# Performance work log

Hardware: AMD Instinct MI355X
Metric: run time of the kernel (lower is better)

Reference implementation:

```python
import jax, jax.numpy as jnp
import numpy as np

B, T, D, H = 8, 1024, 512, 8
HD = D // H  # head_dim = 64


def conv1d(x, w, b):
    # x: [B, C_in, T], w: [C_out, C_in, 3], 'same' padding
    y = jax.lax.conv_general_dilated(x, w, (1,), [(1, 1)],
                                     dimension_numbers=('NCH', 'OIH', 'NCH'))
    return y + b[None, :, None]


def setup_inputs() -> dict:
    key = jax.random.key(0)
    ks = jax.random.split(key, 9)
    s = 0.05
    return {
        'x': jax.random.normal(ks[0], (B, T, D), dtype=jnp.float32),
        'w11': jax.random.normal(ks[1], (D, D, 3), dtype=jnp.float32) * s,
        'b11': jnp.zeros((D,), dtype=jnp.float32),
        'w12': jax.random.normal(ks[2], (D, D, 3), dtype=jnp.float32) * s,
        'b12': jnp.zeros((D,), dtype=jnp.float32),
        'w13': jax.random.normal(ks[3], (D, D, 3), dtype=jnp.float32) * s,
        'b13': jnp.zeros((D,), dtype=jnp.float32),
        'w2': jax.random.normal(ks[4], (D, 2 * D, 3), dtype=jnp.float32) * s,
        'b2': jnp.zeros((D,), dtype=jnp.float32),
    }


def reference(x, w11, b11, w12, b12, w13, b13, w2, b2):
    # dropout is identity in eval mode
    b, t, d = x.shape
    xc = jnp.transpose(x, (0, 2, 1))  # [B, D, T]

    def proj(w, bb):
        y = jax.nn.relu(conv1d(xc, w, bb))        # [B, D, T]
        y = jnp.transpose(y, (0, 2, 1))           # [B, T, D]
        return y.reshape(b, t, H, HD)             # [B, T, H, HD]

    q = proj(w11, b11)
    k = proj(w12, b12)
    v = proj(w13, b13)

    # ---- time-wise attention (d_k = head_dim) ----
    qf = jnp.transpose(q, (0, 2, 1, 3))  # [B, H, T, HD]
    kf = jnp.transpose(k, (0, 2, 1, 3))
    vf = jnp.transpose(v, (0, 2, 1, 3))
    sf = jnp.einsum('bhtd,bhsd->bhts', qf, kf) / np.sqrt(HD)  # [B,H,T,T]
    af = jax.nn.softmax(sf, axis=-1)
    valuesf = jnp.einsum('bhts,bhsd->bhtd', af, vf)           # [B,H,T,HD]
    valuesf = jnp.transpose(valuesf, (0, 2, 1, 3)).reshape(b, t, H * HD)

    # ---- channel-wise attention (d_k = T, scores over head_dim) ----
    qt = jnp.transpose(q, (0, 2, 3, 1))  # [B, H, HD, T]
    kt = jnp.transpose(k, (0, 2, 3, 1))
    vt = jnp.transpose(v, (0, 2, 3, 1))
    st = jnp.einsum('bhct,bhdt->bhcd', qt, kt) / np.sqrt(t)   # [B,H,HD,HD]
    at = jax.nn.softmax(st, axis=-1)
    valuest = jnp.einsum('bhcd,bhdt->bhct', at, vt)           # [B,H,HD,T]
    # torch: permute(0,2,3,1).reshape(B, T, H*HD)
    valuest = jnp.transpose(valuest, (0, 2, 3, 1)).reshape(b, t, H * HD)

    values = jnp.concatenate([valuesf, valuest], axis=-1)     # [B, T, 2D]
    values = jnp.transpose(values, (0, 2, 1))                 # [B, 2D, T]
    out = jax.nn.relu(conv1d(values, w2, b2))                 # [B, D, T]
    return jnp.transpose(out, (0, 2, 1))                      # [B, T, D]
```

## Files before the change

kernel.cpp:

```cpp
#include <hip/hip_runtime.h>

#define BB 8
#define TT 1024
#define DD 512
#define DD2 1024
#define HH 8
#define HDIM 64
#define TP (TT + 2)

typedef short short8 __attribute__((ext_vector_type(8)));
typedef float floatx4 __attribute__((ext_vector_type(4)));

typedef const __attribute__((address_space(1))) unsigned int* gas_ptr;
typedef __attribute__((address_space(3))) unsigned int* las_ptr;

__device__ __forceinline__ unsigned short f2bf(float f) {
    union { float f; unsigned u; } v; v.f = f;
    unsigned r = v.u + 0x7fffu + ((v.u >> 16) & 1u);
    return (unsigned short)(r >> 16);
}

__device__ __forceinline__ void gl2lds16(const void* g, void* l) {
    __builtin_amdgcn_global_load_lds((gas_ptr)g, (las_ptr)l, 16, 0, 0);
}

#define NX4BLK 4104
#define NW1BLK 9216
#define NW2BLK 6144
#define NZBLK 1024
__global__ void k_prep(const float* __restrict__ x, const float* __restrict__ w0,
                       const float* __restrict__ w1, const float* __restrict__ w2,
                       const float* __restrict__ wo,
                       unsigned short* __restrict__ xp, unsigned short* __restrict__ wqkv,
                       unsigned short* __restrict__ w2k, unsigned short* __restrict__ vp,
                       float* __restrict__ gbuf) {
    int blk = blockIdx.x;
    if (blk < NX4BLK) {
        int idx = blk * 256 + threadIdx.x;
        int c4 = idx % (DD / 4);
        int rt = idx / (DD / 4);
        int row = rt % TP;
        int b = rt / TP;
        ushort4 o = {0, 0, 0, 0};
        if (row >= 1 && row <= TT) {
            float4 vv = *(const float4*)&x[((size_t)(b * TT + row - 1)) * DD + c4 * 4];
            o.x = f2bf(vv.x); o.y = f2bf(vv.y); o.z = f2bf(vv.z); o.w = f2bf(vv.w);
        }
        *(ushort4*)&xp[(size_t)idx * 4] = o;
        return;
    }
    blk -= NX4BLK;
    if (blk < NW1BLK) {
        int idx = blk * 256 + threadIdx.x;
        int e = idx & 7;
        int lane = (idx >> 3) & 63;
        int co0 = (idx >> 9) & 31;
        int ci0 = (idx >> 14) & 15;
        int rest = idx >> 18;
        int k = rest % 3, p = rest / 3;
        int co = co0 * 16 + (lane & 15);
        int ci = ci0 * 32 + (lane >> 4) * 8 + e;
        const float* w = (p == 0) ? w0 : ((p == 1) ? w1 : w2);
        wqkv[idx] = f2bf(w[(co * DD + ci) * 3 + k]);
        return;
    }
    blk -= NW1BLK;
    if (blk < NW2BLK) {
        int idx = blk * 256 + threadIdx.x;
        int e = idx & 7;
        int lane = (idx >> 3) & 63;
        int co0 = (idx >> 9) & 31;
        int ci0 = (idx >> 14) & 31;
        int k = idx >> 19;
        int co = co0 * 16 + (lane & 15);
        int ci = ci0 * 32 + (lane >> 4) * 8 + e;
        w2k[idx] = f2bf(wo[(co * DD2 + ci) * 3 + k]);
        return;
    }
    blk -= NW2BLK;
    {
        int idx = blk * 256 + threadIdx.x;
        if (idx < BB * 2 * 2 * DD) {
            int c = idx % (2 * DD);
            int t1 = idx / (2 * DD);
            int row = (t1 & 1) ? (TT + 1) : 0;
            int b = t1 >> 1;
            vp[(b * TP + row) * (2 * DD) + c] = 0;
        }
        if (idx < 64 * HDIM * HDIM) gbuf[idx] = 0.f;
    }
}

__global__ __launch_bounds__(256) void k_qkv_conv(
    const unsigned short* __restrict__ xp, const unsigned short* __restrict__ wfrag,
    const float* __restrict__ b11, const float* __restrict__ b12, const float* __restrict__ b13,
    unsigned short* __restrict__ q, unsigned short* __restrict__ qt,
    unsigned short* __restrict__ kfrag, unsigned short* __restrict__ kt,
    unsigned short* __restrict__ v, unsigned short* __restrict__ vtfrag) {
    __shared__ short As[2][80 * 32];
    int wave = threadIdx.x >> 6, lane = threadIdx.x & 63;
    int l15 = lane & 15, quad = lane >> 4;
    int tb = blockIdx.x * 64;
    int cb = blockIdx.y * 128;
    int proj = blockIdx.z % 3, b = blockIdx.z / 3;
    const short* A = (const short*)xp + b * TP * DD;
    const short* WF = (const short*)wfrag + (size_t)proj * 786432 + lane * 8;
    int srow = lane >> 2;
    int scs = (((lane & 3) ^ ((lane >> 3) & 3)) << 3);
    int co0b = (cb >> 4) + wave * 2;

    floatx4 acc[4][2];
#pragma unroll
    for (int mi = 0; mi < 4; ++mi)
#pragma unroll
        for (int ni = 0; ni < 2; ++ni) acc[mi][ni] = (floatx4){0.f, 0.f, 0.f, 0.f};

    auto stage = [&](int it) {
        short* dst = As[it & 1];
        int cib = it * 32;
        for (int j = wave; j < 5; j += 4)
            gl2lds16(A + (tb + j * 16 + srow) * DD + cib + scs, &dst[j * 512]);
    };

    stage(0);
    __syncthreads();

    for (int it = 0; it < 16; ++it) {
        if (it < 15) stage(it + 1);
        const short* Asb = As[it & 1];
        short8 bf[3][2];
#pragma unroll
        for (int k = 0; k < 3; ++k)
#pragma unroll
            for (int ni = 0; ni < 2; ++ni)
                bf[k][ni] = *(const short8*)(WF + ((size_t)((k * 16 + it) * 32 + co0b + ni) << 9));
#pragma unroll
        for (int k = 0; k < 3; ++k) {
            short8 af[4];
#pragma unroll
            for (int mi = 0; mi < 4; ++mi) {
                int arow = mi * 16 + l15 + k;
                af[mi] = *(const short8*)&Asb[arow * 32 + ((quad ^ ((arow >> 1) & 3)) << 3)];
            }
#pragma unroll
            for (int mi = 0; mi < 4; ++mi)
#pragma unroll
                for (int ni = 0; ni < 2; ++ni)
                    acc[mi][ni] = __builtin_amdgcn_mfma_f32_16x16x32_bf16(af[mi], bf[k][ni], acc[mi][ni], 0, 0, 0);
        }
        __syncthreads();
    }

    const float* bias = (proj == 0) ? b11 : ((proj == 1) ? b12 : b13);
#pragma unroll
    for (int ni = 0; ni < 2; ++ni) {
        int co = cb + wave * 32 + ni * 16 + l15;
        float bv = bias[co];
        int h = co >> 6, hd = co & 63;
        int bh = b * HH + h;
#pragma unroll
        for (int mi = 0; mi < 4; ++mi) {
            int tbase = tb + mi * 16 + quad * 4;
            unsigned short bb[4];
            ushort4 pk;
#pragma unroll
            for (int r = 0; r < 4; ++r) {
                float val = fmaxf(acc[mi][ni][r] + bv, 0.f);
                bb[r] = f2bf(val);
                ((unsigned short*)&pk)[r] = bb[r];
            }
            if (proj == 0) {
#pragma unroll
                for (int r = 0; r < 4; ++r)
                    q[((size_t)bh * TT + tbase + r) * HDIM + hd] = bb[r];
                *(ushort4*)&qt[((size_t)bh * HDIM + hd) * TT + tbase] = pk;
            } else if (proj == 1) {
                *(ushort4*)&kt[((size_t)bh * HDIM + hd) * TT + tbase] = pk;
                int sblk = tbase >> 6;
                int jr = (quad & 1) + 2 * (mi >> 1);
                int l15a_base = 4 * (quad >> 1) + 8 * (mi & 1);
                int kf = hd >> 5, quad_a = (hd >> 3) & 3, elem = hd & 7;
                size_t base = ((((size_t)bh * 16 + sblk) * 4 + jr) * 2 + kf) * 512 +
                              quad_a * 128 + elem;
#pragma unroll
                for (int r = 0; r < 4; ++r)
                    kfrag[base + (l15a_base + r) * 8] = bb[r];
            } else {
#pragma unroll
                for (int r = 0; r < 4; ++r)
                    v[((size_t)bh * TT + tbase + r) * HDIM + hd] = bb[r];
                int sblk = tbase >> 6;
                int df = hd >> 4, l15a = hd & 15;
                int kf = mi >> 1;
                int quad_a = 2 * (mi & 1) + (quad >> 1);
                int elem = (quad & 1) * 4;
                size_t base = ((((size_t)bh * 16 + sblk) * 4 + df) * 2 + kf) * 512 +
                              (quad_a * 16 + l15a) * 8 + elem;
                *(ushort4*)&vtfrag[base] = pk;
            }
        }
    }
}

__global__ __launch_bounds__(256) void k_attn_gram(
    const unsigned short* __restrict__ q, const unsigned short* __restrict__ kfrag,
    const unsigned short* __restrict__ vtfrag, const unsigned short* __restrict__ qt,
    const unsigned short* __restrict__ kt, float* __restrict__ gbuf,
    unsigned short* __restrict__ vp) {
    int wave = threadIdx.x >> 6, lane = threadIdx.x & 63;
    int l15 = lane & 15, quad = lane >> 4;
    int bh = blockIdx.y;

    if (blockIdx.x < 16) {
        int b = bh >> 3, h = bh & 7;
        int qr = blockIdx.x * 64 + wave * 16;
        const short* Q = (const short*)q + (size_t)bh * TT * HDIM;
        const short* KF = (const short*)kfrag + (size_t)bh * 16 * 8 * 512 + lane * 8;
        const short* VF = (const short*)vtfrag + (size_t)bh * 16 * 8 * 512 + lane * 8;

        short8 bq[2];
#pragma unroll
        for (int kf = 0; kf < 2; ++kf)
            bq[kf] = *(const short8*)(Q + (qr + l15) * HDIM + kf * 32 + quad * 8);

        floatx4 o[4];
#pragma unroll
        for (int df = 0; df < 4; ++df) o[df] = (floatx4){0.f, 0.f, 0.f, 0.f};
        float lacc = 0.f;

        for (int sblk = 0; sblk < 16; ++sblk) {
            const short* kp = KF + sblk * 8 * 512;
            const short* vv = VF + sblk * 8 * 512;
            floatx4 c[4];
#pragma unroll
            for (int jr = 0; jr < 4; ++jr) c[jr] = (floatx4){0.f, 0.f, 0.f, 0.f};
#pragma unroll
            for (int jr = 0; jr < 4; ++jr) {
#pragma unroll
                for (int kf = 0; kf < 2; ++kf) {
                    short8 ak = *(const short8*)(kp + (jr * 2 + kf) * 512);
                    c[jr] = __builtin_amdgcn_mfma_f32_16x16x32_bf16(ak, bq[kf], c[jr], 0, 0, 0);
                }
            }
            short8 pb[2];
#pragma unroll
            for (int kf = 0; kf < 2; ++kf) {
                union { short8 s; unsigned u[4]; } pk;
#pragma unroll
                for (int half = 0; half < 2; ++half) {
                    floatx4 cc = c[2 * kf + half];
                    float p0 = __expf(cc[0] * 0.125f);
                    float p1 = __expf(cc[1] * 0.125f);
                    float p2 = __expf(cc[2] * 0.125f);
                    float p3 = __expf(cc[3] * 0.125f);
                    lacc += (p0 + p1) + (p2 + p3);
                    pk.u[half * 2] =
                        __builtin_amdgcn_perm(__float_as_uint(p1), __float_as_uint(p0), 0x07060302u);
                    pk.u[half * 2 + 1] =
                        __builtin_amdgcn_perm(__float_as_uint(p3), __float_as_uint(p2), 0x07060302u);
                }
                pb[kf] = pk.s;
            }
#pragma unroll
            for (int df = 0; df < 4; ++df) {
#pragma unroll
                for (int kf = 0; kf < 2; ++kf) {
                    short8 av = *(const short8*)(vv + (df * 2 + kf) * 512);
                    o[df] = __builtin_amdgcn_mfma_f32_16x16x32_bf16(av, pb[kf], o[df], 0, 0, 0);
                }
            }
        }

        lacc += __shfl_xor(lacc, 16);
        lacc += __shfl_xor(lacc, 32);
        float linv = 1.f / lacc;

        unsigned short* vrow = vp + (size_t)(b * TP + 1 + qr + l15) * (2 * DD) + h * 64;
#pragma unroll
        for (int df = 0; df < 4; ++df) {
            ushort4 pk;
#pragma unroll
            for (int r = 0; r < 4; ++r) ((unsigned short*)&pk)[r] = f2bf(o[df][r] * linv);
            *(ushort4*)&vrow[df * 16 + quad * 4] = pk;
        }
    } else {
        int tc = blockIdx.x - 16;
        const short* Qt = (const short*)qt + (size_t)bh * HDIM * TT;
        const short* Kt = (const short*)kt + (size_t)bh * HDIM * TT;

        floatx4 g[4];
#pragma unroll
        for (int nt = 0; nt < 4; ++nt) g[nt] = (floatx4){0.f, 0.f, 0.f, 0.f};

        int t0b = tc * 256;
        for (int t0 = 0; t0 < 256; t0 += 32) {
            short8 aq = *(const short8*)(Qt + (wave * 16 + l15) * TT + t0b + t0 + quad * 8);
#pragma unroll
            for (int nt = 0; nt < 4; ++nt) {
                short8 bk = *(const short8*)(Kt + (nt * 16 + l15) * TT + t0b + t0 + quad * 8);
                g[nt] = __builtin_amdgcn_mfma_f32_16x16x32_bf16(aq, bk, g[nt], 0, 0, 0);
            }
        }
        float* gb = gbuf + bh * HDIM * HDIM;
#pragma unroll
        for (int nt = 0; nt < 4; ++nt) {
#pragma unroll
            for (int r = 0; r < 4; ++r) {
                int row = wave * 16 + quad * 4 + r;
                atomicAdd(&gb[row * HDIM + nt * 16 + l15], g[nt][r]);
            }
        }
    }
}

__global__ __launch_bounds__(256) void k_chan_av(
    const float* __restrict__ gbuf, const unsigned short* __restrict__ v,
    unsigned short* __restrict__ vp) {
    __shared__ short lds_a[64 * 64];
    int wave = threadIdx.x >> 6, lane = threadIdx.x & 63;
    int l15 = lane & 15, quad = lane >> 4;
    int tc = blockIdx.x, bh = blockIdx.y;
    int b = bh >> 3, h = bh & 7;
    const float sc = 0.03125f;

    if (threadIdx.x < 64) {
        const float* gb = gbuf + bh * HDIM * HDIM + threadIdx.x * HDIM;
        float mx = -3.0e38f;
        for (int j = 0; j < 64; ++j) mx = fmaxf(mx, gb[j] * sc);
        float sum = 0.f;
        for (int j = 0; j < 64; ++j) sum += __expf(gb[j] * sc - mx);
        float inv = 1.f / sum;
        for (int j = 0; j < 64; ++j)
            lds_a[threadIdx.x * 64 + j] = (short)f2bf(__expf(gb[j] * sc - mx) * inv);
    }
    __syncthreads();

    const short* V = (const short*)v + (size_t)bh * TT * HDIM;
    short8 pa[2];
#pragma unroll
    for (int kf = 0; kf < 2; ++kf)
        pa[kf] = *(const short8*)&lds_a[(wave * 16 + l15) * 64 + kf * 32 + quad * 8];

    for (int tt = 0; tt < 16; ++tt) {
        int ttile = tc * 16 + tt;
        floatx4 c = (floatx4){0.f, 0.f, 0.f, 0.f};
#pragma unroll
        for (int kf = 0; kf < 2; ++kf) {
            short8 bv = *(const short8*)(V + (ttile * 16 + l15) * HDIM + kf * 32 + quad * 8);
            c = __builtin_amdgcn_mfma_f32_16x16x32_bf16(pa[kf], bv, c, 0, 0, 0);
        }
        int t = ttile * 16 + l15;
#pragma unroll
        for (int r = 0; r < 4; ++r) {
            int crow = wave * 16 + quad * 4 + r;
            int tout = crow * 16 + (t >> 6);
            int col = 512 + ((t & 63) << 3) + h;
            vp[(b * TP + 1 + tout) * (2 * DD) + col] = f2bf(c[r]);
        }
    }
}

__global__ __launch_bounds__(256) void k_out_conv(
    const unsigned short* __restrict__ vp, const unsigned short* __restrict__ w2k,
    const float* __restrict__ b2, float* __restrict__ out) {
    __shared__ short As[2][144 * 64];
    int wave = threadIdx.x >> 6, lane = threadIdx.x & 63;
    int l15 = lane & 15, quad = lane >> 4;
    int wm = wave >> 1, wn = wave & 1;
    int tb = blockIdx.x * 128;
    int cb = blockIdx.y * 64;
    int b = blockIdx.z;
    const short* A = (const short*)vp + b * TP * DD2;
    const short* WF = (const short*)w2k + lane * 8;
    int srow8 = lane >> 3;
    int scl = ((lane & 7) ^ srow8) * 8;
    int co0b = (cb >> 4) + wn * 2;

    floatx4 acc[4][2];
#pragma unroll
    for (int mi = 0; mi < 4; ++mi)
#pragma unroll
        for (int ni = 0; ni < 2; ++ni) acc[mi][ni] = (floatx4){0.f, 0.f, 0.f, 0.f};

    auto stage = [&](int it) {
        short* dst = As[it & 1];
        int cib = it * 64;
        for (int g = wave; g < 18; g += 4) {
            int j = g >> 1, hf = g & 1;
            int row = hf * 8 + srow8;
            gl2lds16(A + (tb + j * 16 + row) * DD2 + cib + scl, &dst[j * 1024 + hf * 512]);
        }
    };

    stage(0);
    __syncthreads();

    for (int it = 0; it < 16; ++it) {
        if (it < 15) stage(it + 1);
        const short* Asb = As[it & 1];
#pragma unroll
        for (int k = 0; k < 3; ++k) {
            short8 bf[2][2];
#pragma unroll
            for (int kfh = 0; kfh < 2; ++kfh)
#pragma unroll
                for (int ni = 0; ni < 2; ++ni)
                    bf[kfh][ni] = *(const short8*)(WF +
                        ((size_t)((k * 32 + it * 2 + kfh) * 32 + co0b + ni) << 9));
#pragma unroll
            for (int kfh = 0; kfh < 2; ++kfh) {
                short8 af[4];
#pragma unroll
                for (int mi = 0; mi < 4; ++mi) {
                    int arow = wm * 64 + mi * 16 + l15 + k;
                    int cl = kfh * 4 + quad;
                    af[mi] = *(const short8*)&Asb[arow * 64 + ((cl ^ (arow & 7)) << 3)];
                }
#pragma unroll
                for (int mi = 0; mi < 4; ++mi)
#pragma unroll
                    for (int ni = 0; ni < 2; ++ni)
                        acc[mi][ni] = __builtin_amdgcn_mfma_f32_16x16x32_bf16(af[mi], bf[kfh][ni], acc[mi][ni], 0, 0, 0);
            }
        }
        __syncthreads();
    }

#pragma unroll
    for (int ni = 0; ni < 2; ++ni) {
        int co = cb + wn * 32 + ni * 16 + l15;
        float bv = b2[co];
#pragma unroll
        for (int mi = 0; mi < 4; ++mi) {
#pragma unroll
            for (int r = 0; r < 4; ++r) {
                int t = tb + wm * 64 + mi * 16 + quad * 4 + r;
                out[((size_t)b * TT + t) * DD + co] = fmaxf(acc[mi][ni][r] + bv, 0.f);
            }
        }
    }
}

extern "C" void kernel_launch(void* const* d_in, const int* in_sizes, int n_in,
                              void* d_out, int out_size, void* d_ws, size_t ws_size,
                              hipStream_t stream) {
    const float* x = (const float*)d_in[0];
    const float* w11 = (const float*)d_in[1];
    const float* b11 = (const float*)d_in[2];
    const float* w12 = (const float*)d_in[3];
    const float* b12 = (const float*)d_in[4];
    const float* w13 = (const float*)d_in[5];
    const float* b13 = (const float*)d_in[6];
    const float* w2 = (const float*)d_in[7];
    const float* b2 = (const float*)d_in[8];
    float* out = (float*)d_out;

    char* ws = (char*)d_ws;
    size_t off = 0;
    auto alloc = [&](size_t bytes) {
        void* p = ws + off;
        off += (bytes + 255) & ~(size_t)255;
        return p;
    };
    unsigned short* xp = (unsigned short*)alloc((size_t)BB * TP * DD * 2);
    unsigned short* wqkv = (unsigned short*)alloc((size_t)9 * DD * DD * 2);
    unsigned short* w2k = (unsigned short*)alloc((size_t)3 * DD * DD2 * 2);
    unsigned short* q = (unsigned short*)alloc((size_t)BB * HH * TT * HDIM * 2);
    unsigned short* qt = (unsigned short*)alloc((size_t)BB * HH * TT * HDIM * 2);
    unsigned short* kfrag = (unsigned short*)alloc((size_t)BB * HH * TT * HDIM * 2);
    unsigned short* kt = (unsigned short*)alloc((size_t)BB * HH * TT * HDIM * 2);
    unsigned short* v = (unsigned short*)alloc((size_t)BB * HH * TT * HDIM * 2);
    unsigned short* vtfrag = (unsigned short*)alloc((size_t)BB * HH * TT * HDIM * 2);
    float* gbuf = (float*)alloc((size_t)64 * HDIM * HDIM * 4);
    unsigned short* vp = (unsigned short*)alloc((size_t)BB * TP * 2 * DD * 2);
    (void)alloc(65536);

    k_prep<<<NX4BLK + NW1BLK + NW2BLK + NZBLK, 256, 0, stream>>>(x, w11, w12, w13, w2,
                                                                 xp, wqkv, w2k, vp, gbuf);
    k_qkv_conv<<<dim3(TT / 64, DD / 128, BB * 3), 256, 0, stream>>>(xp, wqkv, b11, b12, b13,
                                                                    q, qt, kfrag, kt, v, vtfrag);
    k_attn_gram<<<dim3(20, BB * HH), 256, 0, stream>>>(q, kfrag, vtfrag, qt, kt, gbuf, vp);
    k_chan_av<<<dim3(4, BB * HH), 256, 0, stream>>>(gbuf, v, vp);
    k_out_conv<<<dim3(TT / 128, DD / 64, BB), 256, 0, stream>>>(vp, w2k, b2, out);
}
```

Measured before the change: 236.2 us.

## Double time tile in QKV conv and stage K/V fragments through LDS in attention

The QKV conv kernel now computes 128 time steps per block instead of 64, so each wave reuses its weight fragments across eight M-tiles, and the fragment index math is adjusted to match. The time-wise attention branch now double-buffers K and V fragment blocks in shared memory with async global-to-LDS loads, replacing direct global reads shared by the four waves. This aims to cut weight and K/V global traffic. In exchange it uses more registers and LDS, launches fewer conv blocks, and adds a barrier on every attention iteration.

```diff
diff --git a/kernel.cpp b/kernel.cpp
--- a/kernel.cpp
+++ b/kernel.cpp
@@ -97,10 +97,10 @@
     unsigned short* __restrict__ q, unsigned short* __restrict__ qt,
     unsigned short* __restrict__ kfrag, unsigned short* __restrict__ kt,
     unsigned short* __restrict__ v, unsigned short* __restrict__ vtfrag) {
-    __shared__ short As[2][80 * 32];
+    __shared__ short As[2][144 * 32];
     int wave = threadIdx.x >> 6, lane = threadIdx.x & 63;
     int l15 = lane & 15, quad = lane >> 4;
-    int tb = blockIdx.x * 64;
+    int tb = blockIdx.x * 128;
     int cb = blockIdx.y * 128;
     int proj = blockIdx.z % 3, b = blockIdx.z / 3;
     const short* A = (const short*)xp + b * TP * DD;
@@ -109,16 +109,16 @@
     int scs = (((lane & 3) ^ ((lane >> 3) & 3)) << 3);
     int co0b = (cb >> 4) + wave * 2;
 
-    floatx4 acc[4][2];
-#pragma unroll
-    for (int mi = 0; mi < 4; ++mi)
+    floatx4 acc[8][2];
+#pragma unroll
+    for (int mi = 0; mi < 8; ++mi)
 #pragma unroll
         for (int ni = 0; ni < 2; ++ni) acc[mi][ni] = (floatx4){0.f, 0.f, 0.f, 0.f};
 
     auto stage = [&](int it) {
         short* dst = As[it & 1];
         int cib = it * 32;
-        for (int j = wave; j < 5; j += 4)
+        for (int j = wave; j < 9; j += 4)
             gl2lds16(A + (tb + j * 16 + srow) * DD + cib + scs, &dst[j * 512]);
     };
 
@@ -136,17 +136,13 @@
                 bf[k][ni] = *(const short8*)(WF + ((size_t)((k * 16 + it) * 32 + co0b + ni) << 9));
 #pragma unroll
         for (int k = 0; k < 3; ++k) {
-            short8 af[4];
-#pragma unroll
-            for (int mi = 0; mi < 4; ++mi) {
+#pragma unroll
+            for (int mi = 0; mi < 8; ++mi) {
                 int arow = mi * 16 + l15 + k;
-                af[mi] = *(const short8*)&Asb[arow * 32 + ((quad ^ ((arow >> 1) & 3)) << 3)];
-            }
-#pragma unroll
-            for (int mi = 0; mi < 4; ++mi)
-#pragma unroll
-                for (int ni = 0; ni < 2; ++ni)
-                    acc[mi][ni] = __builtin_amdgcn_mfma_f32_16x16x32_bf16(af[mi], bf[k][ni], acc[mi][ni], 0, 0, 0);
+                short8 af = *(const short8*)&Asb[arow * 32 + ((quad ^ ((arow >> 1) & 3)) << 3)];
+                acc[mi][0] = __builtin_amdgcn_mfma_f32_16x16x32_bf16(af, bf[k][0], acc[mi][0], 0, 0, 0);
+                acc[mi][1] = __builtin_amdgcn_mfma_f32_16x16x32_bf16(af, bf[k][1], acc[mi][1], 0, 0, 0);
+            }
         }
         __syncthreads();
     }
@@ -159,7 +155,7 @@
         int h = co >> 6, hd = co & 63;
         int bh = b * HH + h;
 #pragma unroll
-        for (int mi = 0; mi < 4; ++mi) {
+        for (int mi = 0; mi < 8; ++mi) {
             int tbase = tb + mi * 16 + quad * 4;
             unsigned short bb[4];
             ushort4 pk;
@@ -177,7 +173,7 @@
             } else if (proj == 1) {
                 *(ushort4*)&kt[((size_t)bh * HDIM + hd) * TT + tbase] = pk;
                 int sblk = tbase >> 6;
-                int jr = (quad & 1) + 2 * (mi >> 1);
+                int jr = (quad & 1) + 2 * ((mi >> 1) & 1);
                 int l15a_base = 4 * (quad >> 1) + 8 * (mi & 1);
                 int kf = hd >> 5, quad_a = (hd >> 3) & 3, elem = hd & 7;
                 size_t base = ((((size_t)bh * 16 + sblk) * 4 + jr) * 2 + kf) * 512 +
@@ -191,7 +187,7 @@
                     v[((size_t)bh * TT + tbase + r) * HDIM + hd] = bb[r];
                 int sblk = tbase >> 6;
                 int df = hd >> 4, l15a = hd & 15;
-                int kf = mi >> 1;
+                int kf = (mi >> 1) & 1;
                 int quad_a = 2 * (mi & 1) + (quad >> 1);
                 int elem = (quad & 1) * 4;
                 size_t base = ((((size_t)bh * 16 + sblk) * 4 + df) * 2 + kf) * 512 +
@@ -207,6 +203,7 @@
     const unsigned short* __restrict__ vtfrag, const unsigned short* __restrict__ qt,
     const unsigned short* __restrict__ kt, float* __restrict__ gbuf,
     unsigned short* __restrict__ vp) {
+    __shared__ short kvs[2][8192];
     int wave = threadIdx.x >> 6, lane = threadIdx.x & 63;
     int l15 = lane & 15, quad = lane >> 4;
     int bh = blockIdx.y;
@@ -228,9 +225,21 @@
         for (int df = 0; df < 4; ++df) o[df] = (floatx4){0.f, 0.f, 0.f, 0.f};
         float lacc = 0.f;
 
+        auto stagekv = [&](int s) {
+            short* dst = kvs[s & 1];
+            for (int f = wave; f < 8; f += 4) {
+                gl2lds16(KF + s * 4096 + f * 512, &dst[f * 512]);
+                gl2lds16(VF + s * 4096 + f * 512, &dst[4096 + f * 512]);
+            }
+        };
+
+        stagekv(0);
+        __syncthreads();
+
         for (int sblk = 0; sblk < 16; ++sblk) {
-            const short* kp = KF + sblk * 8 * 512;
-            const short* vv = VF + sblk * 8 * 512;
+            if (sblk < 15) stagekv(sblk + 1);
+            const short* kb = (const short*)&kvs[sblk & 1][0] + lane * 8;
+            const short* vb = kb + 4096;
             floatx4 c[4];
 #pragma unroll
             for (int jr = 0; jr < 4; ++jr) c[jr] = (floatx4){0.f, 0.f, 0.f, 0.f};
@@ -238,7 +247,7 @@
             for (int jr = 0; jr < 4; ++jr) {
 #pragma unroll
                 for (int kf = 0; kf < 2; ++kf) {
-                    short8 ak = *(const short8*)(kp + (jr * 2 + kf) * 512);
+                    short8 ak = *(const short8*)(kb + (jr * 2 + kf) * 512);
                     c[jr] = __builtin_amdgcn_mfma_f32_16x16x32_bf16(ak, bq[kf], c[jr], 0, 0, 0);
                 }
             }
@@ -265,10 +274,11 @@
             for (int df = 0; df < 4; ++df) {
 #pragma unroll
                 for (int kf = 0; kf < 2; ++kf) {
-                    short8 av = *(const short8*)(vv + (df * 2 + kf) * 512);
+                    short8 av = *(const short8*)(vb + (df * 2 + kf) * 512);
                     o[df] = __builtin_amdgcn_mfma_f32_16x16x32_bf16(av, pb[kf], o[df], 0, 0, 0);
                 }
             }
+            __syncthreads();
         }
 
         lacc += __shfl_xor(lacc, 16);
@@ -477,8 +487,8 @@
 
     k_prep<<<NX4BLK + NW1BLK + NW2BLK + NZBLK, 256, 0, stream>>>(x, w11, w12, w13, w2,
                                                                  xp, wqkv, w2k, vp, gbuf);
-    k_qkv_conv<<<dim3(TT / 64, DD / 128, BB * 3), 256, 0, stream>>>(xp, wqkv, b11, b12, b13,
-                                                                    q, qt, kfrag, kt, v, vtfrag);
+    k_qkv_conv<<<dim3(TT / 128, DD / 128, BB * 3), 256, 0, stream>>>(xp, wqkv, b11, b12, b13,
+                                                                     q, qt, kfrag, kt, v, vtfrag);
     k_attn_gram<<<dim3(20, BB * HH), 256, 0, stream>>>(q, kfrag, vtfrag, qt, kt, gbuf, vp);
     k_chan_av<<<dim3(4, BB * HH), 256, 0, stream>>>(gbuf, v, vp);
     k_out_conv<<<dim3(TT / 128, DD / 64, BB), 256, 0, stream>>>(vp, w2k, b2, out);
```

After: 228.3 us. 3.4% less time.

## Widen QKV conv K-step to 64 and stage attention K/V tiles in LDS

Applied to the files above, without the earlier changes.

The QKV convolution kernel now stages 64 input channels per iteration instead of 32, using a new XOR swizzle. This halves the number of loop iterations and barriers, and weight fragments are loaded per tap. The time-wise attention kernel now double-buffers the per-block K and V fragments through LDS via global_load_lds, so the four waves share one copy instead of each reading from global memory. This adds LDS usage and an extra barrier per s-block, which may reduce occupancy.

```diff
diff --git a/kernel.cpp b/kernel.cpp
--- a/kernel.cpp
+++ b/kernel.cpp
@@ -97,7 +97,7 @@
     unsigned short* __restrict__ q, unsigned short* __restrict__ qt,
     unsigned short* __restrict__ kfrag, unsigned short* __restrict__ kt,
     unsigned short* __restrict__ v, unsigned short* __restrict__ vtfrag) {
-    __shared__ short As[2][80 * 32];
+    __shared__ short As[2][80 * 64];
     int wave = threadIdx.x >> 6, lane = threadIdx.x & 63;
     int l15 = lane & 15, quad = lane >> 4;
     int tb = blockIdx.x * 64;
@@ -105,8 +105,8 @@
     int proj = blockIdx.z % 3, b = blockIdx.z / 3;
     const short* A = (const short*)xp + b * TP * DD;
     const short* WF = (const short*)wfrag + (size_t)proj * 786432 + lane * 8;
-    int srow = lane >> 2;
-    int scs = (((lane & 3) ^ ((lane >> 3) & 3)) << 3);
+    int srow8 = lane >> 3;
+    int scl = ((lane & 7) ^ srow8) * 8;
     int co0b = (cb >> 4) + wave * 2;
 
     floatx4 acc[4][2];
@@ -117,36 +117,44 @@
 
     auto stage = [&](int it) {
         short* dst = As[it & 1];
-        int cib = it * 32;
-        for (int j = wave; j < 5; j += 4)
-            gl2lds16(A + (tb + j * 16 + srow) * DD + cib + scs, &dst[j * 512]);
+        int cib = it * 64;
+        for (int g = wave; g < 10; g += 4) {
+            int j = g >> 1, hf = g & 1;
+            int row = hf * 8 + srow8;
+            gl2lds16(A + (tb + j * 16 + row) * DD + cib + scl, &dst[j * 1024 + hf * 512]);
+        }
     };
 
     stage(0);
     __syncthreads();
 
-    for (int it = 0; it < 16; ++it) {
-        if (it < 15) stage(it + 1);
+    for (int it = 0; it < 8; ++it) {
+        if (it < 7) stage(it + 1);
         const short* Asb = As[it & 1];
-        short8 bf[3][2];
-#pragma unroll
-        for (int k = 0; k < 3; ++k)
-#pragma unroll
-            for (int ni = 0; ni < 2; ++ni)
-                bf[k][ni] = *(const short8*)(WF + ((size_t)((k * 16 + it) * 32 + co0b + ni) << 9));
 #pragma unroll
         for (int k = 0; k < 3; ++k) {
-            short8 af[4];
-#pragma unroll
-            for (int mi = 0; mi < 4; ++mi) {
-                int arow = mi * 16 + l15 + k;
-                af[mi] = *(const short8*)&Asb[arow * 32 + ((quad ^ ((arow >> 1) & 3)) << 3)];
-            }
-#pragma unroll
-            for (int mi = 0; mi < 4; ++mi)
+            short8 bf[2][2];
+#pragma unroll
+            for (int kf = 0; kf < 2; ++kf)
 #pragma unroll
                 for (int ni = 0; ni < 2; ++ni)
-                    acc[mi][ni] = __builtin_amdgcn_mfma_f32_16x16x32_bf16(af[mi], bf[k][ni], acc[mi][ni], 0, 0, 0);
+                    bf[kf][ni] = *(const short8*)(WF +
+                        ((size_t)((k * 16 + it * 2 + kf) * 32 + co0b + ni) << 9));
+#pragma unroll
+            for (int kf = 0; kf < 2; ++kf) {
+                short8 af[4];
+#pragma unroll
+                for (int mi = 0; mi < 4; ++mi) {
+                    int arow = mi * 16 + l15 + k;
+                    int cl = kf * 4 + quad;
+                    af[mi] = *(const short8*)&Asb[arow * 64 + ((cl ^ (arow & 7)) << 3)];
+                }
+#pragma unroll
+                for (int mi = 0; mi < 4; ++mi)
+#pragma unroll
+                    for (int ni = 0; ni < 2; ++ni)
+                        acc[mi][ni] = __builtin_amdgcn_mfma_f32_16x16x32_bf16(af[mi], bf[kf][ni], acc[mi][ni], 0, 0, 0);
+            }
         }
         __syncthreads();
     }
@@ -207,6 +215,7 @@
     const unsigned short* __restrict__ vtfrag, const unsigned short* __restrict__ qt,
     const unsigned short* __restrict__ kt, float* __restrict__ gbuf,
     unsigned short* __restrict__ vp) {
+    __shared__ short kvs[2][8192];
     int wave = threadIdx.x >> 6, lane = threadIdx.x & 63;
     int l15 = lane & 15, quad = lane >> 4;
     int bh = blockIdx.y;
@@ -228,9 +237,21 @@
         for (int df = 0; df < 4; ++df) o[df] = (floatx4){0.f, 0.f, 0.f, 0.f};
         float lacc = 0.f;
 
+        auto stagekv = [&](int s) {
+            short* dst = kvs[s & 1];
+            for (int f = wave; f < 8; f += 4) {
+                gl2lds16(KF + s * 4096 + f * 512, &dst[f * 512]);
+                gl2lds16(VF + s * 4096 + f * 512, &dst[4096 + f * 512]);
+            }
+        };
+
+        stagekv(0);
+        __syncthreads();
+
         for (int sblk = 0; sblk < 16; ++sblk) {
-            const short* kp = KF + sblk * 8 * 512;
-            const short* vv = VF + sblk * 8 * 512;
+            if (sblk < 15) stagekv(sblk + 1);
+            const short* kb = (const short*)&kvs[sblk & 1][0] + lane * 8;
+            const short* vb = kb + 4096;
             floatx4 c[4];
 #pragma unroll
             for (int jr = 0; jr < 4; ++jr) c[jr] = (floatx4){0.f, 0.f, 0.f, 0.f};
@@ -238,7 +259,7 @@
             for (int jr = 0; jr < 4; ++jr) {
 #pragma unroll
                 for (int kf = 0; kf < 2; ++kf) {
-                    short8 ak = *(const short8*)(kp + (jr * 2 + kf) * 512);
+                    short8 ak = *(const short8*)(kb + (jr * 2 + kf) * 512);
                     c[jr] = __builtin_amdgcn_mfma_f32_16x16x32_bf16(ak, bq[kf], c[jr], 0, 0, 0);
                 }
             }
@@ -265,10 +286,11 @@
             for (int df = 0; df < 4; ++df) {
 #pragma unroll
                 for (int kf = 0; kf < 2; ++kf) {
-                    short8 av = *(const short8*)(vv + (df * 2 + kf) * 512);
+                    short8 av = *(const short8*)(vb + (df * 2 + kf) * 512);
                     o[df] = __builtin_amdgcn_mfma_f32_16x16x32_bf16(av, pb[kf], o[df], 0, 0, 0);
                 }
             }
+            __syncthreads();
         }
 
         lacc += __shfl_xor(lacc, 16);
```

Measured after the change: 218.2 us. -7.6%, faster.
